# Kernel optimization log

Measured on AMD Instinct MI355X. Metric: run time of the kernel, lower is better.

The kernel has to match this reference:

```python
import jax, jax.numpy as jnp
import numpy as np

B, N, H, W, P = 32, 6, 512, 512, 512
SCALE, ASPECT, MIN_PH = 0.5, 1.0, 60.0


def setup_inputs() -> dict:
    key = jax.random.key(0)
    k1, k2, k3, k4, k5, k6 = jax.random.split(key, 6)
    images = jax.random.normal(k1, (B, H, W, 3), jnp.float32)
    patch = jax.random.normal(k2, (P, P, 3), jnp.float32)
    # person bboxes (ymin, xmin, ymax, xmax) in pixels, fully inside the image
    hsz = jax.random.uniform(k3, (B, N), jnp.float32, 120.0, 400.0)
    wsz = jax.random.uniform(k4, (B, N), jnp.float32, 120.0, 400.0)
    ymin = jax.random.uniform(k5, (B, N), jnp.float32) * (H - hsz)
    xmin = jax.random.uniform(k6, (B, N), jnp.float32) * (W - wsz)
    boxes = jnp.stack([ymin, xmin, ymin + hsz, xmin + wsz], axis=-1)
    return {"images": images, "boxes": boxes, "patch": patch}


def _patch_boxes(boxes):
    # Patcher.create: derive (ymin_patch, xmin_patch, patch_h, patch_w) from each bbox
    ymin, xmin, ymax, xmax = (boxes[..., 0], boxes[..., 1], boxes[..., 2], boxes[..., 3])
    h = ymax - ymin
    w = xmax - xmin
    pw = h * SCALE
    ph = ASPECT * pw
    oy = ymin + h * 0.5
    ox = xmin + w * 0.5
    yp = jnp.maximum(oy - ph * 0.5, 0.0)
    xp = jnp.maximum(ox - pw * 0.5, 0.0)
    yp = jnp.where(yp + ph > H, H - ph, yp)
    xp = jnp.where(xp + pw > W, W - pw, xp)
    valid = ph > MIN_PH  # ragged filter -> mask
    return jnp.stack([yp, xp, ph, pw], axis=-1), valid


def _paste_one(img, patch, box, valid):
    # fused gather(resize bilinear, half-pixel centers) + scatter of the patch into img
    Pn = patch.shape[0]
    b = box.astype(jnp.int32)  # tf.cast truncation
    y0b, x0b, h, w = b[0], b[1], b[2], b[3]
    hf = jnp.maximum(h, 1).astype(jnp.float32)
    wf = jnp.maximum(w, 1).astype(jnp.float32)
    dy = jnp.arange(img.shape[0]) - y0b
    dx = jnp.arange(img.shape[1]) - x0b
    sy = jnp.clip((dy.astype(jnp.float32) + 0.5) * (Pn / hf) - 0.5, 0.0, Pn - 1.0)
    sx = jnp.clip((dx.astype(jnp.float32) + 0.5) * (Pn / wf) - 0.5, 0.0, Pn - 1.0)
    yl = jnp.floor(sy).astype(jnp.int32); yh = jnp.minimum(yl + 1, Pn - 1); wy = sy - yl
    xl = jnp.floor(sx).astype(jnp.int32); xh = jnp.minimum(xl + 1, Pn - 1); wx = sx - xl
    # separable bilinear: rows [H, P, 3] then cols -> [H, W, 3]
    rows = patch[yl] * (1.0 - wy)[:, None, None] + patch[yh] * wy[:, None, None]
    val = rows[:, xl] * (1.0 - wx)[None, :, None] + rows[:, xh] * wx[None, :, None]
    inside = ((dy >= 0) & (dy < h))[:, None] & ((dx >= 0) & (dx < w))[None, :] & valid
    return jnp.where(inside[..., None], val, img)


def reference(images, boxes, patch):
    pboxes, valid = _patch_boxes(boxes)
    def step(imgs, xs):
        bx, v = xs  # [B,4], [B]
        imgs = jax.vmap(lambda im, b_, v_: _paste_one(im, patch, b_, v_))(imgs, bx, v)
        return imgs, None
    # sequential over patches (later patches overwrite earlier, as in the tf while_loop)
    out, _ = jax.lax.scan(step, images, (jnp.transpose(pboxes, (1, 0, 2)), valid.T))
    return out
```

## Files before the change

kernel.cpp:

```cpp
#include <hip/hip_runtime.h>


#define Bn 32
#define Nn 6
#define Hh 512
#define Ww 512
#define Pp 512

__global__ __launch_bounds__(256) void patch_attack_kernel(
    const float* __restrict__ images,
    const float* __restrict__ boxes,
    const float* __restrict__ patch,
    float* __restrict__ out)
{
    const int pix = blockIdx.x * 256 + threadIdx.x;
    const int b   = blockIdx.x >> 10;
    const int rem = pix & (Hh * Ww - 1);
    const int y   = rem >> 9;
    const int x   = rem & (Ww - 1);

    const float* __restrict__ bx = boxes + (size_t)b * Nn * 4;

    float r0, r1, r2;
    bool covered = false;

    #pragma unroll
    for (int n = Nn - 1; n >= 0; --n) {
        const float ymin = bx[n * 4 + 0];
        const float xmin = bx[n * 4 + 1];
        const float ymax = bx[n * 4 + 2];
        const float xmax = bx[n * 4 + 3];
        const float h  = ymax - ymin;
        const float w  = xmax - xmin;
        const float pw = h * 0.5f;
        const float ph = 1.0f * pw;
        const float oy = ymin + h * 0.5f;
        const float ox = xmin + w * 0.5f;
        float yp = fmaxf(oy - ph * 0.5f, 0.0f);
        float xp = fmaxf(ox - pw * 0.5f, 0.0f);
        yp = (yp + ph > (float)Hh) ? ((float)Hh - ph) : yp;
        xp = (xp + pw > (float)Ww) ? ((float)Ww - pw) : xp;
        const bool valid = ph > 60.0f;

        const int y0b = (int)yp;
        const int x0b = (int)xp;
        const int hI  = (int)ph;
        const int wI  = (int)pw;
        const int dy  = y - y0b;
        const int dx  = x - x0b;

        if (valid && dy >= 0 && dy < hI && dx >= 0 && dx < wI) {
            const float hf = (float)(hI > 1 ? hI : 1);
            const float wf = (float)(wI > 1 ? wI : 1);
            float sy = ((float)dy + 0.5f) * ((float)Pp / hf) - 0.5f;
            float sx = ((float)dx + 0.5f) * ((float)Pp / wf) - 0.5f;
            sy = fminf(fmaxf(sy, 0.0f), (float)(Pp - 1));
            sx = fminf(fmaxf(sx, 0.0f), (float)(Pp - 1));
            const int   yl = (int)floorf(sy);
            const int   yh = (yl + 1 < Pp - 1) ? (yl + 1) : (Pp - 1);
            const float wy = sy - (float)yl;
            const int   xl = (int)floorf(sx);
            const int   xh = (xl + 1 < Pp - 1) ? (xl + 1) : (Pp - 1);
            const float wx = sx - (float)xl;

            const float* __restrict__ pll = patch + ((size_t)yl * Pp + xl) * 3;
            const float* __restrict__ plh = patch + ((size_t)yl * Pp + xh) * 3;
            const float* __restrict__ phl = patch + ((size_t)yh * Pp + xl) * 3;
            const float* __restrict__ phh = patch + ((size_t)yh * Pp + xh) * 3;
            const float omwy = 1.0f - wy;
            const float omwx = 1.0f - wx;
            r0 = (pll[0] * omwy + phl[0] * wy) * omwx + (plh[0] * omwy + phh[0] * wy) * wx;
            r1 = (pll[1] * omwy + phl[1] * wy) * omwx + (plh[1] * omwy + phh[1] * wy) * wx;
            r2 = (pll[2] * omwy + phl[2] * wy) * omwx + (plh[2] * omwy + phh[2] * wy) * wx;
            covered = true;
            break;
        }
    }

    if (!covered) {
        const float* __restrict__ ip = images + (size_t)pix * 3;
        r0 = ip[0];
        r1 = ip[1];
        r2 = ip[2];
    }

    float* __restrict__ op = out + (size_t)pix * 3;
    op[0] = r0;
    op[1] = r1;
    op[2] = r2;
}

extern "C" void kernel_launch(void* const* d_in, const int* in_sizes, int n_in,
                              void* d_out, int out_size, void* d_ws, size_t ws_size,
                              hipStream_t stream) {
    const float* images = (const float*)d_in[0];
    const float* boxes  = (const float*)d_in[1];
    const float* patch  = (const float*)d_in[2];
    float* out = (float*)d_out;

    const int total_pixels = Bn * Hh * Ww;
    const int block = 256;
    const int grid  = total_pixels / block;

    patch_attack_kernel<<<grid, block, 0, stream>>>(images, boxes, patch, out);
}
```

Measured before the change: 188.7 us.

## Process four pixels per thread with vectorized nontemporal loads and stores

```diff
diff --git a/kernel.cpp b/kernel.cpp
--- a/kernel.cpp
+++ b/kernel.cpp
@@ -7,22 +7,24 @@
 #define Ww 512
 #define Pp 512
 
+typedef float f32x4 __attribute__((ext_vector_type(4)));
+
 __global__ __launch_bounds__(256) void patch_attack_kernel(
     const float* __restrict__ images,
     const float* __restrict__ boxes,
     const float* __restrict__ patch,
     float* __restrict__ out)
 {
-    const int pix = blockIdx.x * 256 + threadIdx.x;
-    const int b   = blockIdx.x >> 10;
-    const int rem = pix & (Hh * Ww - 1);
-    const int y   = rem >> 9;
-    const int x   = rem & (Ww - 1);
+    const int chunk = blockIdx.x * 256 + threadIdx.x;
+    const int b     = chunk >> 16;
+    const int rem   = chunk & 65535;
+    const int y     = rem >> 7;
+    const int x4    = (rem & 127) << 2;
 
     const float* __restrict__ bx = boxes + (size_t)b * Nn * 4;
 
-    float r0, r1, r2;
-    bool covered = false;
+    float r[12];
+    bool cov[4] = {false, false, false, false};
 
     #pragma unroll
     for (int n = Nn - 1; n >= 0; --n) {
@@ -47,47 +49,73 @@
         const int hI  = (int)ph;
         const int wI  = (int)pw;
         const int dy  = y - y0b;
-        const int dx  = x - x0b;
 
-        if (valid && dy >= 0 && dy < hI && dx >= 0 && dx < wI) {
-            const float hf = (float)(hI > 1 ? hI : 1);
-            const float wf = (float)(wI > 1 ? wI : 1);
-            float sy = ((float)dy + 0.5f) * ((float)Pp / hf) - 0.5f;
-            float sx = ((float)dx + 0.5f) * ((float)Pp / wf) - 0.5f;
-            sy = fminf(fmaxf(sy, 0.0f), (float)(Pp - 1));
+        if (!(valid && dy >= 0 && dy < hI)) continue;
+
+        const float hf = (float)(hI > 1 ? hI : 1);
+        const float wf = (float)(wI > 1 ? wI : 1);
+        float sy = ((float)dy + 0.5f) * ((float)Pp / hf) - 0.5f;
+        sy = fminf(fmaxf(sy, 0.0f), (float)(Pp - 1));
+        const int   yl = (int)floorf(sy);
+        const int   yh = (yl + 1 < Pp - 1) ? (yl + 1) : (Pp - 1);
+        const float wy = sy - (float)yl;
+        const float omwy = 1.0f - wy;
+        const float winv = (float)Pp / wf;
+        const float* __restrict__ rowl = patch + (size_t)yl * (Pp * 3);
+        const float* __restrict__ rowh = patch + (size_t)yh * (Pp * 3);
+
+        #pragma unroll
+        for (int j = 0; j < 4; ++j) {
+            if (cov[j]) continue;
+            const int dx = x4 + j - x0b;
+            if (dx < 0 || dx >= wI) continue;
+
+            float sx = ((float)dx + 0.5f) * winv - 0.5f;
             sx = fminf(fmaxf(sx, 0.0f), (float)(Pp - 1));
-            const int   yl = (int)floorf(sy);
-            const int   yh = (yl + 1 < Pp - 1) ? (yl + 1) : (Pp - 1);
-            const float wy = sy - (float)yl;
             const int   xl = (int)floorf(sx);
             const int   xh = (xl + 1 < Pp - 1) ? (xl + 1) : (Pp - 1);
             const float wx = sx - (float)xl;
+            const float omwx = 1.0f - wx;
 
-            const float* __restrict__ pll = patch + ((size_t)yl * Pp + xl) * 3;
-            const float* __restrict__ plh = patch + ((size_t)yl * Pp + xh) * 3;
-            const float* __restrict__ phl = patch + ((size_t)yh * Pp + xl) * 3;
-            const float* __restrict__ phh = patch + ((size_t)yh * Pp + xh) * 3;
-            const float omwy = 1.0f - wy;
-            const float omwx = 1.0f - wx;
-            r0 = (pll[0] * omwy + phl[0] * wy) * omwx + (plh[0] * omwy + phh[0] * wy) * wx;
-            r1 = (pll[1] * omwy + phl[1] * wy) * omwx + (plh[1] * omwy + phh[1] * wy) * wx;
-            r2 = (pll[2] * omwy + phl[2] * wy) * omwx + (plh[2] * omwy + phh[2] * wy) * wx;
-            covered = true;
-            break;
+            const float* __restrict__ pll = rowl + xl * 3;
+            const float* __restrict__ plh = rowl + xh * 3;
+            const float* __restrict__ phl = rowh + xl * 3;
+            const float* __restrict__ phh = rowh + xh * 3;
+            r[j * 3 + 0] = (pll[0] * omwy + phl[0] * wy) * omwx + (plh[0] * omwy + phh[0] * wy) * wx;
+            r[j * 3 + 1] = (pll[1] * omwy + phl[1] * wy) * omwx + (plh[1] * omwy + phh[1] * wy) * wx;
+            r[j * 3 + 2] = (pll[2] * omwy + phl[2] * wy) * omwx + (plh[2] * omwy + phh[2] * wy) * wx;
+            cov[j] = true;
+        }
+        if (cov[0] & cov[1] & cov[2] & cov[3]) break;
+    }
+
+    if (!(cov[0] & cov[1] & cov[2] & cov[3])) {
+        const f32x4* __restrict__ ip =
+            (const f32x4*)(images + (size_t)chunk * 12);
+        const f32x4 i0 = __builtin_nontemporal_load(ip + 0);
+        const f32x4 i1 = __builtin_nontemporal_load(ip + 1);
+        const f32x4 i2 = __builtin_nontemporal_load(ip + 2);
+        const float img[12] = {i0.x, i0.y, i0.z, i0.w,
+                               i1.x, i1.y, i1.z, i1.w,
+                               i2.x, i2.y, i2.z, i2.w};
+        #pragma unroll
+        for (int j = 0; j < 4; ++j) {
+            if (!cov[j]) {
+                r[j * 3 + 0] = img[j * 3 + 0];
+                r[j * 3 + 1] = img[j * 3 + 1];
+                r[j * 3 + 2] = img[j * 3 + 2];
+            }
         }
     }
 
-    if (!covered) {
-        const float* __restrict__ ip = images + (size_t)pix * 3;
-        r0 = ip[0];
-        r1 = ip[1];
-        r2 = ip[2];
-    }
-
-    float* __restrict__ op = out + (size_t)pix * 3;
-    op[0] = r0;
-    op[1] = r1;
-    op[2] = r2;
+    f32x4* __restrict__ op = (f32x4*)(out + (size_t)chunk * 12);
+    f32x4 o0, o1, o2;
+    o0.x = r[0];  o0.y = r[1];  o0.z = r[2];  o0.w = r[3];
+    o1.x = r[4];  o1.y = r[5];  o1.z = r[6];  o1.w = r[7];
+    o2.x = r[8];  o2.y = r[9];  o2.z = r[10]; o2.w = r[11];
+    __builtin_nontemporal_store(o0, op + 0);
+    __builtin_nontemporal_store(o1, op + 1);
+    __builtin_nontemporal_store(o2, op + 2);
 }
 
 extern "C" void kernel_launch(void* const* d_in, const int* in_sizes, int n_in,
@@ -98,9 +126,9 @@
     const float* patch  = (const float*)d_in[2];
     float* out = (float*)d_out;
 
-    const int total_pixels = Bn * Hh * Ww;
+    const int total_chunks = Bn * Hh * Ww / 4;
     const int block = 256;
-    const int grid  = total_pixels / block;
+    const int grid  = total_chunks / block;
 
     patch_attack_kernel<<<grid, block, 0, stream>>>(images, boxes, patch, out);
 }
```

Result: slower. 215.8 us (+14.4%).
